# Kernel tuning notes

Hardware: AMD Instinct MI355X
Metric: run time of the kernel (lower is better)

The kernel has to match this reference:

```python
import jax, jax.numpy as jnp
import numpy as np

NB_POOLS = 256

def setup_inputs() -> dict:
    key = jax.random.key(0)
    x = jax.random.normal(key, (32, 32, 32, 512), dtype=jnp.float32)
    return {"x": x}

def reference(x):
    B, R, C, F = x.shape
    nb_maps = R * C
    # self-correlation: (B, nb_maps, nb_maps), normalized by feature dim
    x3 = x.reshape(B, nb_maps, F)
    corr = jnp.einsum('bmf,bnf->bmn', x3, x3) / F
    corr = corr.reshape(B, R, C, nb_maps)
    # percentile ranks: round(linspace(1, nb_maps-1, nb_pools)) as in tf.lin_space
    ranks = jnp.round(jnp.linspace(1.0, nb_maps - 1, NB_POOLS)).astype(jnp.int32)
    # tf.nn.top_k(k=nb_maps, sorted=True) == full descending sort along last axis
    x_sort = -jnp.sort(-corr, axis=-1)
    # gather selected order statistics -> (B, R, C, nb_pools)
    x_pool = jnp.take(x_sort, ranks, axis=-1)
    return x_pool
```

## Files before the change

kernel.cpp:

```cpp
#include <hip/hip_runtime.h>

#define NB    32
#define NMAPS 1024
#define FDIM  512
#define NPOOL 256

typedef short  bf16x8 __attribute__((ext_vector_type(8)));
typedef float  f32x4  __attribute__((ext_vector_type(4)));

__device__ __forceinline__ unsigned short f2bf(float f) {
  unsigned int u = __float_as_uint(f);
  return (unsigned short)((u + 0x7fffu + ((u >> 16) & 1u)) >> 16);
}

__device__ __forceinline__ int swz(int c) { return c ^ ((c >> 3) & 7); }

__device__ __forceinline__ int rank_of(int o) { return (765 + 2044 * o) / 510; }

__global__ __launch_bounds__(256) void convert_perm_kernel(const float* __restrict__ x,
                                                           unsigned short* __restrict__ xp) {
  const float s = 0.044194173824159216f;
  const int T  = blockIdx.x * 256 + threadIdx.x;
  const int li = T & 15;
  const int kc = (T >> 4) & 63;
  const int g  = (T >> 10) & 63;
  const int b  = T >> 16;
  const float* src = x + ((size_t)((b * 64 + g) * 16 + li) * FDIM + kc * 8);
  const float4 p = *(const float4*)src;
  const float4 q = *(const float4*)(src + 4);
  uint4 o;
  o.x = (unsigned)f2bf(p.x * s) | ((unsigned)f2bf(p.y * s) << 16);
  o.y = (unsigned)f2bf(p.z * s) | ((unsigned)f2bf(p.w * s) << 16);
  o.z = (unsigned)f2bf(q.x * s) | ((unsigned)f2bf(q.y * s) << 16);
  o.w = (unsigned)f2bf(q.z * s) | ((unsigned)f2bf(q.w * s) << 16);
  *(uint4*)(xp + (size_t)T * 8) = o;
}

__device__ __forceinline__ void sort32e(float (&v)[32], const int ll) {
#pragma unroll
  for (int kb = 1; kb <= 4; ++kb) {
    const int k = 1 << kb;
#pragma unroll
    for (int jb = 3; jb >= 0; --jb) {
      if (jb >= kb) continue;
      const int j = 1 << jb;
#pragma unroll
      for (int t = 0; t < 32; ++t) {
        if (t & j) continue;
        const int u = t | j;
        const float a0 = v[t], b0 = v[u];
        if ((t & k) != 0) { v[t] = fminf(a0, b0); v[u] = fmaxf(a0, b0); }
        else              { v[t] = fmaxf(a0, b0); v[u] = fminf(a0, b0); }
      }
    }
  }
  unsigned curM = 0;
#pragma unroll
  for (int kb = 5; kb <= 10; ++kb) {
    const int k = 1 << kb;
    const unsigned m = (kb == 10) ? 0u : ((ll & (k >> 5)) ? 0x80000000u : 0u);
    const unsigned d = curM ^ m;
#pragma unroll
    for (int t = 0; t < 32; ++t)
      v[t] = __int_as_float(__float_as_int(v[t]) ^ (int)d);
    curM = m;
#pragma unroll
    for (int jb = 9; jb >= 5; --jb) {
      if (jb >= kb) continue;
      const int jl = 1 << (jb - 5);
      const bool high = (ll & jl) != 0;
#pragma unroll
      for (int t = 0; t < 32; ++t) {
        float o;
        if (jl == 1)
          o = __int_as_float(__builtin_amdgcn_mov_dpp(__float_as_int(v[t]),
                                                      0xB1, 0xF, 0xF, true));
        else if (jl == 2)
          o = __int_as_float(__builtin_amdgcn_mov_dpp(__float_as_int(v[t]),
                                                      0x4E, 0xF, 0xF, true));
        else
          o = __shfl_xor(v[t], jl, 64);
        v[t] = ((v[t] < o) != high) ? o : v[t];
      }
    }
#pragma unroll
    for (int jb = 4; jb >= 0; --jb) {
      const int j = 1 << jb;
#pragma unroll
      for (int t = 0; t < 32; ++t) {
        if (t & j) continue;
        const int u = t | j;
        const float a0 = v[t], b0 = v[u];
        v[t] = fmaxf(a0, b0);
        v[u] = fminf(a0, b0);
      }
    }
  }
}

__global__ __launch_bounds__(512, 4) void fused_kernel(const unsigned short* __restrict__ xp,
                                                       float* __restrict__ out) {
  __shared__ float ex[16 * 1024];

  const int bid = blockIdx.x;
  const int wk  = (bid & 7) * 128 + (bid >> 3);
  const int b   = wk >> 5;
  const int mt  = wk & 31;
  const int M0  = mt * 32;

  const int tid  = threadIdx.x;
  const int lane = tid & 63;
  const int w    = tid >> 6;
  const int li   = lane & 15;
  const int ll   = lane & 31;
  const int h    = lane >> 5;
  const int kh   = lane >> 4;
  const int rloc = 2 * w + h;

  const unsigned short* __restrict__ Xp = xp + (size_t)b * (NMAPS * FDIM);

  f32x4 acc0[8], acc1[8];
#pragma unroll
  for (int n = 0; n < 8; ++n) {
    acc0[n] = (f32x4){0.f, 0.f, 0.f, 0.f};
    acc1[n] = (f32x4){0.f, 0.f, 0.f, 0.f};
  }

  const unsigned short* pA = Xp + (size_t)(2 * mt) * 8192 + lane * 8;
  const unsigned short* pB = Xp + (size_t)(8 * w) * 8192 + lane * 8;

  for (int kc0 = 0; kc0 < 64; kc0 += 4) {
    const bf16x8 A0 = *(const bf16x8*)(pA + kc0 * 128);
    const bf16x8 A1 = *(const bf16x8*)(pA + 8192 + kc0 * 128);
#pragma unroll
    for (int half = 0; half < 2; ++half) {
      bf16x8 B[4];
#pragma unroll
      for (int n = 0; n < 4; ++n)
        B[n] = *(const bf16x8*)(pB + (size_t)(4 * half + n) * 8192 + kc0 * 128);
#pragma unroll
      for (int n = 0; n < 4; ++n) {
        if (half == 0) {
          acc0[n] = __builtin_amdgcn_mfma_f32_16x16x32_bf16(A0, B[n], acc0[n], 0, 0, 0);
          acc1[n] = __builtin_amdgcn_mfma_f32_16x16x32_bf16(A1, B[n], acc1[n], 0, 0, 0);
        } else {
          acc0[4 + n] = __builtin_amdgcn_mfma_f32_16x16x32_bf16(A0, B[n], acc0[4 + n], 0, 0, 0);
          acc1[4 + n] = __builtin_amdgcn_mfma_f32_16x16x32_bf16(A1, B[n], acc1[4 + n], 0, 0, 0);
        }
      }
    }
  }

  float v0[32], v1[32];

#pragma unroll
  for (int n = 0; n < 8; ++n) {
    const int cw = 32 * w + 4 * n + (li >> 2);
    const int q  = li & 3;
#pragma unroll
    for (int r = 0; r < 4; ++r)
      ex[(4 * kh + r) * 1024 + swz(cw) * 4 + q] = acc0[n][r];
  }
  __syncthreads();
#pragma unroll
  for (int i = 0; i < 8; ++i) {
    const float4 t4 = *(const float4*)(ex + rloc * 1024 + swz(8 * ll + i) * 4);
    v0[4 * i + 0] = t4.x; v0[4 * i + 1] = t4.y;
    v0[4 * i + 2] = t4.z; v0[4 * i + 3] = t4.w;
  }
  __syncthreads();

#pragma unroll
  for (int n = 0; n < 8; ++n) {
    const int cw = 32 * w + 4 * n + (li >> 2);
    const int q  = li & 3;
#pragma unroll
    for (int r = 0; r < 4; ++r)
      ex[(4 * kh + r) * 1024 + swz(cw) * 4 + q] = acc1[n][r];
  }
  __syncthreads();
#pragma unroll
  for (int i = 0; i < 8; ++i) {
    const float4 t4 = *(const float4*)(ex + rloc * 1024 + swz(8 * ll + i) * 4);
    v1[4 * i + 0] = t4.x; v1[4 * i + 1] = t4.y;
    v1[4 * i + 2] = t4.z; v1[4 * i + 3] = t4.w;
  }

  sort32e(v0, ll);
#pragma unroll
  for (int i = 0; i < 8; ++i)
    *(float4*)(ex + rloc * 1024 + swz(8 * ll + i) * 4) =
        make_float4(v0[4 * i + 0], v0[4 * i + 1], v0[4 * i + 2], v0[4 * i + 3]);
#pragma unroll
  for (int h2 = 0; h2 < 2; ++h2) {
    const float* sb = ex + (2 * w + h2) * 1024;
    float ov[4];
#pragma unroll
    for (int q = 0; q < 4; ++q) {
      const int s = rank_of(4 * lane + q);
      ov[q] = sb[swz(s >> 2) * 4 + (s & 3)];
    }
    *(float4*)(out + ((size_t)b * NMAPS + M0 + 2 * w + h2) * NPOOL + 4 * lane) =
        make_float4(ov[0], ov[1], ov[2], ov[3]);
  }

  sort32e(v1, ll);
#pragma unroll
  for (int i = 0; i < 8; ++i)
    *(float4*)(ex + rloc * 1024 + swz(8 * ll + i) * 4) =
        make_float4(v1[4 * i + 0], v1[4 * i + 1], v1[4 * i + 2], v1[4 * i + 3]);
#pragma unroll
  for (int h2 = 0; h2 < 2; ++h2) {
    const float* sb = ex + (2 * w + h2) * 1024;
    float ov[4];
#pragma unroll
    for (int q = 0; q < 4; ++q) {
      const int s = rank_of(4 * lane + q);
      ov[q] = sb[swz(s >> 2) * 4 + (s & 3)];
    }
    *(float4*)(out + ((size_t)b * NMAPS + M0 + 16 + 2 * w + h2) * NPOOL + 4 * lane) =
        make_float4(ov[0], ov[1], ov[2], ov[3]);
  }
}

__device__ __forceinline__ bf16x8 ld_frag_f32(const float* p) {
  const float4 a = *(const float4*)p;
  const float4 b = *(const float4*)(p + 4);
  bf16x8 r;
  r[0] = (short)f2bf(a.x); r[1] = (short)f2bf(a.y);
  r[2] = (short)f2bf(a.z); r[3] = (short)f2bf(a.w);
  r[4] = (short)f2bf(b.x); r[5] = (short)f2bf(b.y);
  r[6] = (short)f2bf(b.z); r[7] = (short)f2bf(b.w);
  return r;
}

__device__ __forceinline__ int swz_ex(int row, int col) {
  return col ^ (((col >> 6) & 15) << 1) ^ (row & 1) ^ (((row >> 2) & 1) << 4);
}

__device__ __forceinline__ void sort1024_desc(float (&v)[64], const int li) {
#pragma unroll
  for (int kb = 1; kb <= 10; ++kb) {
    const int k = 1 << kb;
#pragma unroll
    for (int jb = 9; jb >= 0; --jb) {
      if (jb >= kb) continue;
      const int j = 1 << jb;
      if (jb >= 6) {
        const int jl = j >> 6;
        const bool up = (li & (k >> 6)) != 0;
        const bool tm = up == ((li & jl) == 0);
#pragma unroll
        for (int t = 0; t < 64; ++t) {
          const float o  = __shfl_xor(v[t], jl, 64);
          const float mn = fminf(v[t], o);
          const float mx = fmaxf(v[t], o);
          v[t] = tm ? mn : mx;
        }
      } else if (kb <= 5) {
#pragma unroll
        for (int t = 0; t < 64; ++t) {
          if (t & j) continue;
          const int u = t | j;
          const float a0 = v[t], b0 = v[u];
          if ((t & k) != 0) { v[t] = fminf(a0, b0); v[u] = fmaxf(a0, b0); }
          else              { v[t] = fmaxf(a0, b0); v[u] = fminf(a0, b0); }
        }
      } else {
        const bool tm = (li & (k >> 6)) != 0;
#pragma unroll
        for (int t = 0; t < 64; ++t) {
          if (t & j) continue;
          const int u = t | j;
          const float a0 = v[t], b0 = v[u];
          const float mn = fminf(a0, b0), mx = fmaxf(a0, b0);
          v[t] = tm ? mn : mx;
          v[u] = tm ? mx : mn;
        }
      }
    }
  }
}

__global__ __launch_bounds__(512) void corr_pool_kernel(const float* __restrict__ x,
                                                        float* __restrict__ out) {
  __shared__ float ex[16 * 1024];
  const int bid = blockIdx.x;
  const int xcd = bid & 7;
  const int idx = bid >> 3;
  const int b   = xcd + 8 * (idx >> 5);
  const int M0  = (idx & 31) * 32;

  const int tid  = threadIdx.x;
  const int lane = tid & 63;
  const int w    = tid >> 6;
  const int li   = lane & 15;
  const int kh   = lane >> 4;

  const float* __restrict__ Xf = x + (size_t)b * NMAPS * FDIM;

  f32x4 acc[2][8];
#pragma unroll
  for (int a = 0; a < 2; ++a)
#pragma unroll
    for (int n = 0; n < 8; ++n) acc[a][n] = (f32x4){0.f, 0.f, 0.f, 0.f};

#pragma unroll 2
  for (int k0 = 0; k0 < FDIM; k0 += 32) {
    bf16x8 A[2], B[8];
#pragma unroll
    for (int a = 0; a < 2; ++a)
      A[a] = ld_frag_f32(Xf + (M0 + 16 * a + li) * FDIM + k0 + kh * 8);
#pragma unroll
    for (int n = 0; n < 8; ++n)
      B[n] = ld_frag_f32(Xf + (128 * w + 16 * n + li) * FDIM + k0 + kh * 8);
#pragma unroll
    for (int a = 0; a < 2; ++a)
#pragma unroll
      for (int n = 0; n < 8; ++n)
        acc[a][n] = __builtin_amdgcn_mfma_f32_16x16x32_bf16(A[a], B[n], acc[a][n], 0, 0, 0);
  }

  const int R = 4 * w + kh;
  float v[64];
#pragma unroll
  for (int p = 0; p < 2; ++p) {
#pragma unroll
    for (int n = 0; n < 8; ++n) {
      const int col = 128 * w + 16 * n + li;
#pragma unroll
      for (int r = 0; r < 4; ++r) {
        const int rw = 16 * p + 4 * kh + r;
        ex[(rw & 15) * 1024 + swz_ex(rw, col)] = acc[p][n][r] * (1.0f / FDIM);
      }
    }
    __syncthreads();
    if ((w >> 2) == p) {
#pragma unroll
      for (int t = 0; t < 64; ++t)
        v[t] = ex[(R & 15) * 1024 + swz_ex(R, 64 * li + t)];
    }
    __syncthreads();
  }

  sort1024_desc(v, li);

  __syncthreads();
#pragma unroll
  for (int gp = 0; gp < 2; ++gp) {
    if ((w >> 2) == gp) {
#pragma unroll
      for (int t = 0; t < 64; ++t)
        ex[(R & 15) * 1024 + swz_ex(R, 64 * li + t)] = v[t];
    }
    __syncthreads();
    if ((w >> 2) == gp) {
#pragma unroll
      for (int rp = 0; rp < 4; ++rp) {
        const int Rr = 4 * w + rp;
        float ov[4];
#pragma unroll
        for (int q = 0; q < 4; ++q) {
          const int s = rank_of(4 * lane + q);
          ov[q] = ex[(Rr & 15) * 1024 + swz_ex(Rr, s)];
        }
        float* op = out + (size_t)(b * NMAPS + M0 + Rr) * NPOOL;
        *(float4*)(op + 4 * lane) = make_float4(ov[0], ov[1], ov[2], ov[3]);
      }
    }
    __syncthreads();
  }
}

extern "C" void kernel_launch(void* const* d_in, const int* in_sizes, int n_in,
                              void* d_out, int out_size, void* d_ws, size_t ws_size,
                              hipStream_t stream) {
  const float* x = (const float*)d_in[0];
  float* out = (float*)d_out;
  const size_t bf16_bytes = (size_t)NB * NMAPS * FDIM * sizeof(unsigned short);

  if (ws_size >= bf16_bytes) {
    unsigned short* xp = (unsigned short*)d_ws;
    convert_perm_kernel<<<dim3((NB * NMAPS * FDIM) / (256 * 8)), dim3(256), 0, stream>>>(x, xp);
    fused_kernel<<<dim3(NB * 32), dim3(512), 0, stream>>>(xp, out);
  } else {
    corr_pool_kernel<<<dim3(NB * 32), dim3(512), 0, stream>>>(x, out);
  }
}
```

Baseline: 143.7 us.

## Halve rows per block to cut registers/LDS and use ds_swizzle for sort shuffles

Each block now computes a 16-row correlation tile instead of 32. That halves the accumulators, the per-thread sort arrays and the shared-memory buffer, and doubles the grid so more waves can be resident (launch bound raised to 6). All 8 waves sort one row each, staged through LDS in two halves. The sort's cross-lane exchanges at distances 4/8/16 now use ds_swizzle instead of __shfl_xor, which avoids the address computation of bpermute. The trade-off is that each block loads its B tiles for only half as many output rows, so global/L2 traffic for B roughly doubles.

```diff
diff --git a/kernel.cpp b/kernel.cpp
--- a/kernel.cpp
+++ b/kernel.cpp
@@ -36,6 +36,17 @@
   *(uint4*)(xp + (size_t)T * 8) = o;
 }
 
+__device__ __forceinline__ float xsh(float x, const int jl) {
+  const int xi = __float_as_int(x);
+  int r;
+  if (jl == 1)      r = __builtin_amdgcn_mov_dpp(xi, 0xB1, 0xF, 0xF, true);
+  else if (jl == 2) r = __builtin_amdgcn_mov_dpp(xi, 0x4E, 0xF, 0xF, true);
+  else if (jl == 4) r = __builtin_amdgcn_ds_swizzle(xi, 0x101F);
+  else if (jl == 8) r = __builtin_amdgcn_ds_swizzle(xi, 0x201F);
+  else              r = __builtin_amdgcn_ds_swizzle(xi, 0x401F);
+  return __int_as_float(r);
+}
+
 __device__ __forceinline__ void sort32e(float (&v)[32], const int ll) {
 #pragma unroll
   for (int kb = 1; kb <= 4; ++kb) {
@@ -71,15 +82,7 @@
       const bool high = (ll & jl) != 0;
 #pragma unroll
       for (int t = 0; t < 32; ++t) {
-        float o;
-        if (jl == 1)
-          o = __int_as_float(__builtin_amdgcn_mov_dpp(__float_as_int(v[t]),
-                                                      0xB1, 0xF, 0xF, true));
-        else if (jl == 2)
-          o = __int_as_float(__builtin_amdgcn_mov_dpp(__float_as_int(v[t]),
-                                                      0x4E, 0xF, 0xF, true));
-        else
-          o = __shfl_xor(v[t], jl, 64);
+        const float o = xsh(v[t], jl);
         v[t] = ((v[t] < o) != high) ? o : v[t];
       }
     }
@@ -98,15 +101,15 @@
   }
 }
 
-__global__ __launch_bounds__(512, 4) void fused_kernel(const unsigned short* __restrict__ xp,
+__global__ __launch_bounds__(512, 6) void fused_kernel(const unsigned short* __restrict__ xp,
                                                        float* __restrict__ out) {
-  __shared__ float ex[16 * 1024];
+  __shared__ float ex[8 * 1024];
 
   const int bid = blockIdx.x;
-  const int wk  = (bid & 7) * 128 + (bid >> 3);
-  const int b   = wk >> 5;
-  const int mt  = wk & 31;
-  const int M0  = mt * 32;
+  const int wk  = (bid & 7) * 256 + (bid >> 3);
+  const int b   = wk >> 6;
+  const int mt  = wk & 63;
+  const int M0  = mt * 16;
 
   const int tid  = threadIdx.x;
   const int lane = tid & 63;
@@ -115,23 +118,18 @@
   const int ll   = lane & 31;
   const int h    = lane >> 5;
   const int kh   = lane >> 4;
-  const int rloc = 2 * w + h;
 
   const unsigned short* __restrict__ Xp = xp + (size_t)b * (NMAPS * FDIM);
 
-  f32x4 acc0[8], acc1[8];
-#pragma unroll
-  for (int n = 0; n < 8; ++n) {
-    acc0[n] = (f32x4){0.f, 0.f, 0.f, 0.f};
-    acc1[n] = (f32x4){0.f, 0.f, 0.f, 0.f};
-  }
-
-  const unsigned short* pA = Xp + (size_t)(2 * mt) * 8192 + lane * 8;
+  f32x4 acc[8];
+#pragma unroll
+  for (int n = 0; n < 8; ++n) acc[n] = (f32x4){0.f, 0.f, 0.f, 0.f};
+
+  const unsigned short* pA = Xp + (size_t)mt * 8192 + lane * 8;
   const unsigned short* pB = Xp + (size_t)(8 * w) * 8192 + lane * 8;
 
   for (int kc0 = 0; kc0 < 64; kc0 += 4) {
     const bf16x8 A0 = *(const bf16x8*)(pA + kc0 * 128);
-    const bf16x8 A1 = *(const bf16x8*)(pA + 8192 + kc0 * 128);
 #pragma unroll
     for (int half = 0; half < 2; ++half) {
       bf16x8 B[4];
@@ -140,86 +138,97 @@
         B[n] = *(const bf16x8*)(pB + (size_t)(4 * half + n) * 8192 + kc0 * 128);
 #pragma unroll
       for (int n = 0; n < 4; ++n) {
-        if (half == 0) {
-          acc0[n] = __builtin_amdgcn_mfma_f32_16x16x32_bf16(A0, B[n], acc0[n], 0, 0, 0);
-          acc1[n] = __builtin_amdgcn_mfma_f32_16x16x32_bf16(A1, B[n], acc1[n], 0, 0, 0);
-        } else {
-          acc0[4 + n] = __builtin_amdgcn_mfma_f32_16x16x32_bf16(A0, B[n], acc0[4 + n], 0, 0, 0);
-          acc1[4 + n] = __builtin_amdgcn_mfma_f32_16x16x32_bf16(A1, B[n], acc1[4 + n], 0, 0, 0);
-        }
-      }
-    }
-  }
-
-  float v0[32], v1[32];
-
-#pragma unroll
-  for (int n = 0; n < 8; ++n) {
-    const int cw = 32 * w + 4 * n + (li >> 2);
-    const int q  = li & 3;
-#pragma unroll
-    for (int r = 0; r < 4; ++r)
-      ex[(4 * kh + r) * 1024 + swz(cw) * 4 + q] = acc0[n][r];
-  }
-  __syncthreads();
-#pragma unroll
-  for (int i = 0; i < 8; ++i) {
-    const float4 t4 = *(const float4*)(ex + rloc * 1024 + swz(8 * ll + i) * 4);
-    v0[4 * i + 0] = t4.x; v0[4 * i + 1] = t4.y;
-    v0[4 * i + 2] = t4.z; v0[4 * i + 3] = t4.w;
-  }
-  __syncthreads();
-
-#pragma unroll
-  for (int n = 0; n < 8; ++n) {
-    const int cw = 32 * w + 4 * n + (li >> 2);
-    const int q  = li & 3;
-#pragma unroll
-    for (int r = 0; r < 4; ++r)
-      ex[(4 * kh + r) * 1024 + swz(cw) * 4 + q] = acc1[n][r];
-  }
-  __syncthreads();
-#pragma unroll
-  for (int i = 0; i < 8; ++i) {
-    const float4 t4 = *(const float4*)(ex + rloc * 1024 + swz(8 * ll + i) * 4);
-    v1[4 * i + 0] = t4.x; v1[4 * i + 1] = t4.y;
-    v1[4 * i + 2] = t4.z; v1[4 * i + 3] = t4.w;
-  }
-
-  sort32e(v0, ll);
-#pragma unroll
-  for (int i = 0; i < 8; ++i)
-    *(float4*)(ex + rloc * 1024 + swz(8 * ll + i) * 4) =
-        make_float4(v0[4 * i + 0], v0[4 * i + 1], v0[4 * i + 2], v0[4 * i + 3]);
-#pragma unroll
-  for (int h2 = 0; h2 < 2; ++h2) {
-    const float* sb = ex + (2 * w + h2) * 1024;
-    float ov[4];
-#pragma unroll
-    for (int q = 0; q < 4; ++q) {
-      const int s = rank_of(4 * lane + q);
-      ov[q] = sb[swz(s >> 2) * 4 + (s & 3)];
-    }
-    *(float4*)(out + ((size_t)b * NMAPS + M0 + 2 * w + h2) * NPOOL + 4 * lane) =
-        make_float4(ov[0], ov[1], ov[2], ov[3]);
-  }
-
-  sort32e(v1, ll);
-#pragma unroll
-  for (int i = 0; i < 8; ++i)
-    *(float4*)(ex + rloc * 1024 + swz(8 * ll + i) * 4) =
-        make_float4(v1[4 * i + 0], v1[4 * i + 1], v1[4 * i + 2], v1[4 * i + 3]);
-#pragma unroll
-  for (int h2 = 0; h2 < 2; ++h2) {
-    const float* sb = ex + (2 * w + h2) * 1024;
-    float ov[4];
-#pragma unroll
-    for (int q = 0; q < 4; ++q) {
-      const int s = rank_of(4 * lane + q);
-      ov[q] = sb[swz(s >> 2) * 4 + (s & 3)];
-    }
-    *(float4*)(out + ((size_t)b * NMAPS + M0 + 16 + 2 * w + h2) * NPOOL + 4 * lane) =
-        make_float4(ov[0], ov[1], ov[2], ov[3]);
+        if (half == 0) acc[n]     = __builtin_amdgcn_mfma_f32_16x16x32_bf16(A0, B[n], acc[n], 0, 0, 0);
+        else           acc[4 + n] = __builtin_amdgcn_mfma_f32_16x16x32_bf16(A0, B[n], acc[4 + n], 0, 0, 0);
+      }
+    }
+  }
+
+  float v[32];
+
+  if (kh < 2) {
+#pragma unroll
+    for (int n = 0; n < 8; ++n) {
+      const int cw = 32 * w + 4 * n + (li >> 2);
+      const int q  = li & 3;
+#pragma unroll
+      for (int r = 0; r < 4; ++r)
+        ex[(4 * kh + r) * 1024 + swz(cw) * 4 + q] = acc[n][r];
+    }
+  }
+  __syncthreads();
+  if (w < 4) {
+    const float* sb = ex + (2 * w + h) * 1024;
+#pragma unroll
+    for (int i = 0; i < 8; ++i) {
+      const float4 t4 = *(const float4*)(sb + swz(8 * ll + i) * 4);
+      v[4 * i + 0] = t4.x; v[4 * i + 1] = t4.y;
+      v[4 * i + 2] = t4.z; v[4 * i + 3] = t4.w;
+    }
+  }
+  __syncthreads();
+  if (kh >= 2) {
+#pragma unroll
+    for (int n = 0; n < 8; ++n) {
+      const int cw = 32 * w + 4 * n + (li >> 2);
+      const int q  = li & 3;
+#pragma unroll
+      for (int r = 0; r < 4; ++r)
+        ex[(4 * (kh - 2) + r) * 1024 + swz(cw) * 4 + q] = acc[n][r];
+    }
+  }
+  __syncthreads();
+  if (w >= 4) {
+    const float* sb = ex + (2 * (w - 4) + h) * 1024;
+#pragma unroll
+    for (int i = 0; i < 8; ++i) {
+      const float4 t4 = *(const float4*)(sb + swz(8 * ll + i) * 4);
+      v[4 * i + 0] = t4.x; v[4 * i + 1] = t4.y;
+      v[4 * i + 2] = t4.z; v[4 * i + 3] = t4.w;
+    }
+  }
+  __syncthreads();
+
+  sort32e(v, ll);
+
+  if (w < 4) {
+    float* sb = ex + (2 * w + h) * 1024;
+#pragma unroll
+    for (int i = 0; i < 8; ++i)
+      *(float4*)(sb + swz(8 * ll + i) * 4) =
+          make_float4(v[4 * i + 0], v[4 * i + 1], v[4 * i + 2], v[4 * i + 3]);
+#pragma unroll
+    for (int h2 = 0; h2 < 2; ++h2) {
+      const float* sg = ex + (2 * w + h2) * 1024;
+      float ov[4];
+#pragma unroll
+      for (int q = 0; q < 4; ++q) {
+        const int s = rank_of(4 * lane + q);
+        ov[q] = sg[swz(s >> 2) * 4 + (s & 3)];
+      }
+      *(float4*)(out + ((size_t)b * NMAPS + M0 + 2 * w + h2) * NPOOL + 4 * lane) =
+          make_float4(ov[0], ov[1], ov[2], ov[3]);
+    }
+  }
+  __syncthreads();
+  if (w >= 4) {
+    float* sb = ex + (2 * (w - 4) + h) * 1024;
+#pragma unroll
+    for (int i = 0; i < 8; ++i)
+      *(float4*)(sb + swz(8 * ll + i) * 4) =
+          make_float4(v[4 * i + 0], v[4 * i + 1], v[4 * i + 2], v[4 * i + 3]);
+#pragma unroll
+    for (int h2 = 0; h2 < 2; ++h2) {
+      const float* sg = ex + (2 * (w - 4) + h2) * 1024;
+      float ov[4];
+#pragma unroll
+      for (int q = 0; q < 4; ++q) {
+        const int s = rank_of(4 * lane + q);
+        ov[q] = sg[swz(s >> 2) * 4 + (s & 3)];
+      }
+      *(float4*)(out + ((size_t)b * NMAPS + M0 + 8 + 2 * (w - 4) + h2) * NPOOL + 4 * lane) =
+          make_float4(ov[0], ov[1], ov[2], ov[3]);
+    }
   }
 }
 
@@ -382,7 +391,7 @@
   if (ws_size >= bf16_bytes) {
     unsigned short* xp = (unsigned short*)d_ws;
     convert_perm_kernel<<<dim3((NB * NMAPS * FDIM) / (256 * 8)), dim3(256), 0, stream>>>(x, xp);
-    fused_kernel<<<dim3(NB * 32), dim3(512), 0, stream>>>(xp, out);
+    fused_kernel<<<dim3(NB * 64), dim3(512), 0, stream>>>(xp, out);
   } else {
     corr_pool_kernel<<<dim3(NB * 32), dim3(512), 0, stream>>>(x, out);
   }
```

Measured after the change: 162.3 us. 13.0% more time.
